# Performance work log

Hardware: AMD Instinct MI355X
Metric: run time of the kernel (lower is better)

Reference implementation:

```python
import jax, jax.numpy as jnp
import numpy as np

B, F, D = 16384, 256, 128
H = [512, 256]
OUT = 8
VOCAB = 100000


def setup_inputs() -> dict:
    key = jax.random.key(0)
    ks = jax.random.split(key, 16)
    s = lambda k, *sh: jax.random.normal(k, sh, jnp.float32) * 0.05
    return dict(
        features=jax.random.normal(ks[0], (B, F), jnp.float32),
        ent_idx=jax.random.randint(ks[1], (B,), 0, VOCAB),
        target=jax.random.randint(ks[2], (B,), 0, OUT),
        Wf=s(ks[3], F, D), bf=jnp.zeros((D,), jnp.float32),
        Wu=s(ks[4], D, D), bu=jnp.zeros((D,), jnp.float32),
        w_cf=s(ks[5], D), w_fc=s(ks[6], D),
        w_ef=s(ks[7], D), w_fe=s(ks[8], D),
        b_c=jnp.zeros((1,), jnp.float32), b_e=jnp.zeros((1,), jnp.float32),
        head_tab=s(ks[9], VOCAB, D), ent_tab=s(ks[10], VOCAB, D),
        W0=s(ks[11], 2 * D, H[0]), b0=jnp.zeros((H[0],), jnp.float32),
        W1=s(ks[12], H[0], H[1]), b1=jnp.zeros((H[1],), jnp.float32),
        W2=s(ks[13], H[1], OUT), b2=jnp.zeros((OUT,), jnp.float32),
    )


def cross_compress(f, e, w_cf, w_fc, w_ef, w_fe, b_c, b_e):
    # torch code builds c = f (outer) e of shape (B,D,D) then matmuls a (D,1)
    # vector; algebraically (f e^T) w = f * (e . w), so we use the O(B*D) form.
    ew_cf = e @ w_cf  # (B,)
    fw_fc = f @ w_fc
    ew_ef = e @ w_ef
    fw_fe = f @ w_fe
    new_f = f * ew_cf[:, None] + e * fw_fc[:, None] + b_c
    new_e = f * ew_ef[:, None] + e * fw_fe[:, None] + b_e
    return new_f, new_e


def reference(features, ent_idx, target, Wf, bf, Wu, bu, w_cf, w_fc, w_ef,
              w_fe, b_c, b_e, head_tab, ent_tab, W0, b0, W1, b1, W2, b2):
    # 'rec' branch of CompanyOperationEvaluation.forward (eval mode, dropout=id)
    cf = jax.nn.relu(features @ Wf + bf)          # feature_layer
    e = ent_tab[ent_idx]                           # entity_embed lookup
    h = head_tab[ent_idx]                          # head_embed lookup (same ids)
    for _ in range(2):
        cf = jax.nn.relu(cf @ Wu + bu)             # user_low_mlp_layer
        h, e = cross_compress(h, e, w_cf, w_fc, w_ef, w_fe, b_c, b_e)
    high = jnp.concatenate([cf, e], axis=1)        # (B, 2D)
    x = jax.nn.relu(high @ W0 + b0)
    x = jax.nn.relu(x @ W1 + b1)
    x = jax.nn.relu(x @ W2 + b2)                   # pred_last_layer
    prob = jax.nn.softmax(x, axis=1)
    return (prob, target)
```

## Files before the change

### kernel.cpp

```cpp
#include <hip/hip_runtime.h>
#include <hip/hip_bf16.h>


typedef __bf16 bf16x8 __attribute__((ext_vector_type(8)));
typedef float floatx4 __attribute__((ext_vector_type(4)));

__device__ __forceinline__ unsigned short f2bf(float x) {
  unsigned int u = __builtin_bit_cast(unsigned int, x);
  u = (u + 0x7FFFu + ((u >> 16) & 1u)) >> 16;
  return (unsigned short)u;
}

__global__ __launch_bounds__(256) void prep_kernel(
    const int* __restrict__ ent_idx, const float* __restrict__ head_tab,
    const float* __restrict__ ent_tab,
    const float* __restrict__ w_cf, const float* __restrict__ w_fc,
    const float* __restrict__ w_ef, const float* __restrict__ w_fe,
    const float* __restrict__ b_c, const float* __restrict__ b_e,
    const float* __restrict__ Wf, const float* __restrict__ Wu,
    const float* __restrict__ W0, const float* __restrict__ W1,
    const float* __restrict__ W2,
    unsigned short* __restrict__ high,
    unsigned short* __restrict__ wfT, unsigned short* __restrict__ wuT,
    unsigned short* __restrict__ w0T, unsigned short* __restrict__ w1T,
    unsigned short* __restrict__ w2T) {
  __shared__ unsigned short tile[32][34];
  const int bid = blockIdx.x, tid = threadIdx.x;
  if (bid < 2048) {
    const int row = bid * 8 + (tid >> 5);
    const int c = (tid & 31) * 4;
    const int idx = ent_idx[row];
    float4 hv = *(const float4*)(head_tab + (size_t)idx * 128 + c);
    float4 ev = *(const float4*)(ent_tab + (size_t)idx * 128 + c);
    float h[4] = {hv.x, hv.y, hv.z, hv.w};
    float e[4] = {ev.x, ev.y, ev.z, ev.w};
    float wcf[4], wfc[4], wef[4], wfe[4];
#pragma unroll
    for (int j = 0; j < 4; ++j) {
      wcf[j] = w_cf[c + j]; wfc[j] = w_fc[c + j];
      wef[j] = w_ef[c + j]; wfe[j] = w_fe[c + j];
    }
    const float bc = b_c[0], be = b_e[0];
#pragma unroll
    for (int it = 0; it < 2; ++it) {
      float d0 = 0, d1 = 0, d2 = 0, d3 = 0;
#pragma unroll
      for (int j = 0; j < 4; ++j) {
        d0 += e[j] * wcf[j]; d1 += h[j] * wfc[j];
        d2 += e[j] * wef[j]; d3 += h[j] * wfe[j];
      }
#pragma unroll
      for (int s = 1; s < 32; s <<= 1) {
        d0 += __shfl_xor(d0, s); d1 += __shfl_xor(d1, s);
        d2 += __shfl_xor(d2, s); d3 += __shfl_xor(d3, s);
      }
      float nh[4], ne[4];
#pragma unroll
      for (int j = 0; j < 4; ++j) {
        nh[j] = h[j] * d0 + e[j] * d1 + bc;
        ne[j] = h[j] * d2 + e[j] * d3 + be;
      }
#pragma unroll
      for (int j = 0; j < 4; ++j) { h[j] = nh[j]; e[j] = ne[j]; }
    }
    uint2 v;
    v.x = (unsigned)f2bf(e[0]) | ((unsigned)f2bf(e[1]) << 16);
    v.y = (unsigned)f2bf(e[2]) | ((unsigned)f2bf(e[3]) << 16);
    *(uint2*)(high + (size_t)row * 256 + 128 + c) = v;
  } else if (bid < 2352) {
    int t = bid - 2048;
    const float* src; unsigned short* dst; int N, K, kt, nt;
    if (t < 32)       { src = Wf; dst = wfT; N = 128; K = 256; kt = t >> 2;       nt = t & 3; }
    else if (t < 48)  { t -= 32;  src = Wu; dst = wuT; N = 128; K = 128; kt = t >> 2; nt = t & 3; }
    else if (t < 176) { t -= 48;  src = W0; dst = w0T; N = 512; K = 256; kt = t >> 4; nt = t & 15; }
    else              { t -= 176; src = W1; dst = w1T; N = 256; K = 512; kt = t >> 3; nt = t & 7; }
    {
      int r = tid >> 3, cg = (tid & 7) * 4;
      float4 v = *(const float4*)(src + (size_t)(kt * 32 + r) * N + nt * 32 + cg);
      tile[r][cg + 0] = f2bf(v.x); tile[r][cg + 1] = f2bf(v.y);
      tile[r][cg + 2] = f2bf(v.z); tile[r][cg + 3] = f2bf(v.w);
    }
    __syncthreads();
    {
      int rp = tid >> 3, cg = (tid & 7) * 4;
      uint2 o;
      o.x = (unsigned)tile[cg + 0][rp] | ((unsigned)tile[cg + 1][rp] << 16);
      o.y = (unsigned)tile[cg + 2][rp] | ((unsigned)tile[cg + 3][rp] << 16);
      *(uint2*)(dst + (size_t)(nt * 32 + rp) * K + kt * 32 + cg) = o;
    }
  } else {
#pragma unroll
    for (int i = 0; i < 8; ++i) {
      int g = tid * 8 + i, k = g >> 3, n = g & 7;
      w2T[n * 256 + k] = f2bf(W2[g]);
    }
  }
}

template <int LDA>
__device__ __forceinline__ void layer_acc(const unsigned short* A_sh,
                                          const unsigned short* __restrict__ BT,
                                          int K, unsigned short* b_sh,
                                          floatx4 acc[2][4]) {
  const int tid = threadIdx.x, lane = tid & 63, wave = tid >> 6;
  const int wm = wave >> 1, wn = wave & 1;
  const int m16 = lane & 15, quad = lane >> 4;
#pragma unroll
  for (int mi = 0; mi < 2; ++mi)
#pragma unroll
    for (int ni = 0; ni < 4; ++ni) acc[mi][ni] = (floatx4){0.f, 0.f, 0.f, 0.f};
  for (int k0 = 0; k0 < K; k0 += 64) {
    __syncthreads();
#pragma unroll
    for (int i = 0; i < 4; ++i) {
      int chunk = i * 256 + tid;
      int row = chunk >> 3, seg = chunk & 7;
      *(uint4*)&b_sh[row * 72 + seg * 8] =
          *(const uint4*)(BT + (size_t)row * K + k0 + seg * 8);
    }
    __syncthreads();
#pragma unroll
    for (int kk = 0; kk < 64; kk += 32) {
      bf16x8 a[2], b[4];
#pragma unroll
      for (int mi = 0; mi < 2; ++mi)
        a[mi] = *(const bf16x8*)&A_sh[(wm * 32 + mi * 16 + m16) * LDA + k0 + kk + quad * 8];
#pragma unroll
      for (int ni = 0; ni < 4; ++ni)
        b[ni] = *(const bf16x8*)&b_sh[(wn * 64 + ni * 16 + m16) * 72 + kk + quad * 8];
#pragma unroll
      for (int mi = 0; mi < 2; ++mi)
#pragma unroll
        for (int ni = 0; ni < 4; ++ni)
          acc[mi][ni] = __builtin_amdgcn_mfma_f32_16x16x32_bf16(a[mi], b[ni], acc[mi][ni], 0, 0, 0);
    }
  }
  __syncthreads();
}

__global__ __launch_bounds__(256) void cf_chain_kernel(
    const float* __restrict__ features, const unsigned short* __restrict__ wfT,
    const unsigned short* __restrict__ wuT, const float* __restrict__ bf_,
    const float* __restrict__ bu, unsigned short* __restrict__ high) {
  __shared__ __align__(16) unsigned short feat_sh[64 * 264];
  __shared__ __align__(16) unsigned short buf0[64 * 136];
  __shared__ __align__(16) unsigned short buf1[64 * 136];
  __shared__ __align__(16) unsigned short b_sh[128 * 72];
  const int tid = threadIdx.x;
  const int r0 = blockIdx.x * 64;
#pragma unroll
  for (int i = 0; i < 16; ++i) {
    int row = i * 4 + (tid >> 6);
    int c = (tid & 63) * 4;
    float4 v = *(const float4*)(features + (size_t)(r0 + row) * 256 + c);
    uint2 o;
    o.x = (unsigned)f2bf(v.x) | ((unsigned)f2bf(v.y) << 16);
    o.y = (unsigned)f2bf(v.z) | ((unsigned)f2bf(v.w) << 16);
    *(uint2*)&feat_sh[row * 264 + c] = o;
  }
  const int lane = tid & 63, wave = tid >> 6;
  const int wm = wave >> 1, wn = wave & 1;
  const int m16 = lane & 15, quad = lane >> 4;
  floatx4 acc[2][4];

  layer_acc<264>(feat_sh, wfT, 256, b_sh, acc);
#pragma unroll
  for (int mi = 0; mi < 2; ++mi)
#pragma unroll
    for (int ni = 0; ni < 4; ++ni) {
      int col = wn * 64 + ni * 16 + m16;
      float bv = bf_[col];
#pragma unroll
      for (int r = 0; r < 4; ++r)
        buf0[(wm * 32 + mi * 16 + quad * 4 + r) * 136 + col] =
            f2bf(fmaxf(acc[mi][ni][r] + bv, 0.f));
    }
  layer_acc<136>(buf0, wuT, 128, b_sh, acc);
#pragma unroll
  for (int mi = 0; mi < 2; ++mi)
#pragma unroll
    for (int ni = 0; ni < 4; ++ni) {
      int col = wn * 64 + ni * 16 + m16;
      float bv = bu[col];
#pragma unroll
      for (int r = 0; r < 4; ++r)
        buf1[(wm * 32 + mi * 16 + quad * 4 + r) * 136 + col] =
            f2bf(fmaxf(acc[mi][ni][r] + bv, 0.f));
    }
  layer_acc<136>(buf1, wuT, 128, b_sh, acc);
#pragma unroll
  for (int mi = 0; mi < 2; ++mi)
#pragma unroll
    for (int ni = 0; ni < 4; ++ni) {
      int col = wn * 64 + ni * 16 + m16;
      float bv = bu[col];
#pragma unroll
      for (int r = 0; r < 4; ++r) {
        int row = r0 + wm * 32 + mi * 16 + quad * 4 + r;
        high[(size_t)row * 256 + col] = f2bf(fmaxf(acc[mi][ni][r] + bv, 0.f));
      }
    }
}

__global__ __launch_bounds__(256) void gemm_kernel(
    const unsigned short* __restrict__ A, const unsigned short* __restrict__ BT,
    const float* __restrict__ bias, unsigned short* __restrict__ C,
    int K, int ldc) {
  __shared__ __align__(16) unsigned short a_sh[128 * 72];
  __shared__ __align__(16) unsigned short b_sh[64 * 72];
  const int tid = threadIdx.x;
  const int bn = blockIdx.x, bm = blockIdx.y;
  const int lane = tid & 63;
  const int wave = tid >> 6;
  const int wm = wave & 1, wn = wave >> 1;
  const int m16 = lane & 15, quad = lane >> 4;

  floatx4 acc[4][2];
#pragma unroll
  for (int i = 0; i < 4; ++i)
#pragma unroll
    for (int j = 0; j < 2; ++j) acc[i][j] = (floatx4){0.f, 0.f, 0.f, 0.f};

  for (int k0 = 0; k0 < K; k0 += 64) {
#pragma unroll
    for (int i = 0; i < 4; ++i) {
      int chunk = i * 256 + tid;
      int row = chunk >> 3, seg = chunk & 7;
      *(uint4*)&a_sh[row * 72 + seg * 8] =
          *(const uint4*)(A + (size_t)(bm * 128 + row) * K + k0 + seg * 8);
    }
#pragma unroll
    for (int i = 0; i < 2; ++i) {
      int chunk = i * 256 + tid;
      int row = chunk >> 3, seg = chunk & 7;
      *(uint4*)&b_sh[row * 72 + seg * 8] =
          *(const uint4*)(BT + (size_t)(bn * 64 + row) * K + k0 + seg * 8);
    }
    __syncthreads();
#pragma unroll
    for (int kk = 0; kk < 64; kk += 32) {
      bf16x8 af[4], bfr[2];
#pragma unroll
      for (int mi = 0; mi < 4; ++mi)
        af[mi] = *(const bf16x8*)&a_sh[(wm * 64 + mi * 16 + m16) * 72 + kk + quad * 8];
#pragma unroll
      for (int ni = 0; ni < 2; ++ni)
        bfr[ni] = *(const bf16x8*)&b_sh[(wn * 32 + ni * 16 + m16) * 72 + kk + quad * 8];
#pragma unroll
      for (int mi = 0; mi < 4; ++mi)
#pragma unroll
        for (int ni = 0; ni < 2; ++ni)
          acc[mi][ni] = __builtin_amdgcn_mfma_f32_16x16x32_bf16(
              af[mi], bfr[ni], acc[mi][ni], 0, 0, 0);
    }
    __syncthreads();
  }
#pragma unroll
  for (int mi = 0; mi < 4; ++mi) {
#pragma unroll
    for (int ni = 0; ni < 2; ++ni) {
      int col = bn * 64 + wn * 32 + ni * 16 + m16;
      float bv = bias[col];
#pragma unroll
      for (int r = 0; r < 4; ++r) {
        int row = bm * 128 + wm * 64 + mi * 16 + quad * 4 + r;
        float v = fmaxf(acc[mi][ni][r] + bv, 0.f);
        C[(size_t)row * ldc + col] = f2bf(v);
      }
    }
  }
}

__global__ __launch_bounds__(256) void gemm_w1_final_kernel(
    const unsigned short* __restrict__ x0, const unsigned short* __restrict__ w1T,
    const float* __restrict__ b1, const unsigned short* __restrict__ w2T,
    const float* __restrict__ b2, const int* __restrict__ target,
    float* __restrict__ out) {
  __shared__ __align__(16) unsigned short a_sh[64 * 72];
  __shared__ __align__(16) unsigned short b_sh[256 * 72];
  __shared__ __align__(16) unsigned short x1_sh[64 * 264];
  __shared__ __align__(16) unsigned short w2_sh[2048];
  const int tid = threadIdx.x;
  const int r0 = blockIdx.x * 64;
  *(uint4*)&w2_sh[tid * 8] = *(const uint4*)(w2T + tid * 8);
  const int lane = tid & 63, wave = tid >> 6;
  const int m16 = lane & 15, quad = lane >> 4;
  floatx4 acc[4][4];
#pragma unroll
  for (int mi = 0; mi < 4; ++mi)
#pragma unroll
    for (int ni = 0; ni < 4; ++ni) acc[mi][ni] = (floatx4){0.f, 0.f, 0.f, 0.f};

  for (int k0 = 0; k0 < 512; k0 += 64) {
    __syncthreads();
#pragma unroll
    for (int i = 0; i < 2; ++i) {
      int chunk = i * 256 + tid;
      int row = chunk >> 3, seg = chunk & 7;
      *(uint4*)&a_sh[row * 72 + seg * 8] =
          *(const uint4*)(x0 + (size_t)(r0 + row) * 512 + k0 + seg * 8);
    }
#pragma unroll
    for (int i = 0; i < 8; ++i) {
      int chunk = i * 256 + tid;
      int row = chunk >> 3, seg = chunk & 7;
      *(uint4*)&b_sh[row * 72 + seg * 8] =
          *(const uint4*)(w1T + (size_t)row * 512 + k0 + seg * 8);
    }
    __syncthreads();
#pragma unroll
    for (int kk = 0; kk < 64; kk += 32) {
      bf16x8 a[4], b[4];
#pragma unroll
      for (int mi = 0; mi < 4; ++mi)
        a[mi] = *(const bf16x8*)&a_sh[(mi * 16 + m16) * 72 + kk + quad * 8];
#pragma unroll
      for (int ni = 0; ni < 4; ++ni)
        b[ni] = *(const bf16x8*)&b_sh[(wave * 64 + ni * 16 + m16) * 72 + kk + quad * 8];
#pragma unroll
      for (int mi = 0; mi < 4; ++mi)
#pragma unroll
        for (int ni = 0; ni < 4; ++ni)
          acc[mi][ni] = __builtin_amdgcn_mfma_f32_16x16x32_bf16(a[mi], b[ni], acc[mi][ni], 0, 0, 0);
    }
  }
#pragma unroll
  for (int mi = 0; mi < 4; ++mi)
#pragma unroll
    for (int ni = 0; ni < 4; ++ni) {
      int col = wave * 64 + ni * 16 + m16;
      float bv = b1[col];
#pragma unroll
      for (int r = 0; r < 4; ++r)
        x1_sh[(mi * 16 + quad * 4 + r) * 264 + col] = f2bf(fmaxf(acc[mi][ni][r] + bv, 0.f));
    }
  __syncthreads();
  {
    int row = tid >> 2, q = tid & 3;
    float p[8];
#pragma unroll
    for (int n = 0; n < 8; ++n) p[n] = 0.f;
#pragma unroll
    for (int jb = 0; jb < 8; ++jb) {
      bf16x8 xv = *(const bf16x8*)&x1_sh[row * 264 + q * 64 + jb * 8];
#pragma unroll
      for (int n = 0; n < 8; ++n) {
        bf16x8 wv = *(const bf16x8*)&w2_sh[n * 256 + q * 64 + jb * 8];
#pragma unroll
        for (int j = 0; j < 8; ++j) p[n] += (float)xv[j] * (float)wv[j];
      }
    }
#pragma unroll
    for (int s = 1; s < 4; s <<= 1)
#pragma unroll
      for (int n = 0; n < 8; ++n) p[n] += __shfl_xor(p[n], s);
    if (q == 0) {
      float mx = -1e30f;
#pragma unroll
      for (int n = 0; n < 8; ++n) {
        p[n] = fmaxf(p[n] + b2[n], 0.f);
        mx = fmaxf(mx, p[n]);
      }
      float sum = 0.f;
#pragma unroll
      for (int n = 0; n < 8; ++n) { p[n] = __expf(p[n] - mx); sum += p[n]; }
      const float inv = 1.f / sum;
      const int gr = r0 + row;
      float4 o0 = {p[0] * inv, p[1] * inv, p[2] * inv, p[3] * inv};
      float4 o1 = {p[4] * inv, p[5] * inv, p[6] * inv, p[7] * inv};
      *(float4*)(out + (size_t)gr * 8) = o0;
      *(float4*)(out + (size_t)gr * 8 + 4) = o1;
      out[16384 * 8 + gr] = (float)target[gr];
    }
  }
}

extern "C" void kernel_launch(void* const* d_in, const int* in_sizes, int n_in,
                              void* d_out, int out_size, void* d_ws, size_t ws_size,
                              hipStream_t stream) {
  const float* features = (const float*)d_in[0];
  const int* ent_idx    = (const int*)d_in[1];
  const int* target     = (const int*)d_in[2];
  const float* Wf  = (const float*)d_in[3];
  const float* bf_ = (const float*)d_in[4];
  const float* Wu  = (const float*)d_in[5];
  const float* bu  = (const float*)d_in[6];
  const float* w_cf = (const float*)d_in[7];
  const float* w_fc = (const float*)d_in[8];
  const float* w_ef = (const float*)d_in[9];
  const float* w_fe = (const float*)d_in[10];
  const float* b_c  = (const float*)d_in[11];
  const float* b_e  = (const float*)d_in[12];
  const float* head_tab = (const float*)d_in[13];
  const float* ent_tab  = (const float*)d_in[14];
  const float* W0 = (const float*)d_in[15];
  const float* b0 = (const float*)d_in[16];
  const float* W1 = (const float*)d_in[17];
  const float* b1 = (const float*)d_in[18];
  const float* W2 = (const float*)d_in[19];
  const float* b2 = (const float*)d_in[20];
  float* out = (float*)d_out;

  unsigned short* ws = (unsigned short*)d_ws;
  size_t off = 0;
  auto alloc = [&](size_t n) { unsigned short* p = ws + off; off += n; return p; };
  unsigned short* high = alloc(16384ull * 256);
  unsigned short* x0   = alloc(16384ull * 512);
  unsigned short* wfT  = alloc(32768);
  unsigned short* wuT  = alloc(16384);
  unsigned short* w0T  = alloc(131072);
  unsigned short* w1T  = alloc(131072);
  unsigned short* w2T  = alloc(2048);
  (void)ws_size; (void)in_sizes; (void)n_in; (void)out_size;

  prep_kernel<<<2353, 256, 0, stream>>>(ent_idx, head_tab, ent_tab,
      w_cf, w_fc, w_ef, w_fe, b_c, b_e, Wf, Wu, W0, W1, W2,
      high, wfT, wuT, w0T, w1T, w2T);
  cf_chain_kernel<<<256, 256, 0, stream>>>(features, wfT, wuT, bf_, bu, high);
  gemm_kernel<<<dim3(8, 128), 256, 0, stream>>>(high, w0T, b0, x0, 256, 512);
  gemm_w1_final_kernel<<<256, 256, 0, stream>>>(x0, w1T, b1, w2T, b2, target, out);
}
```

Measured before the change: 196.5 us.

## Retile MLP kernels: 32-row blocks for chain and final, 128x128 GEMM tiles

The cf chain and final W1/W2 kernels now process 32 rows per block instead of 64, which doubles the grid to 512 blocks so the 256-CU GPU gets more parallelism. The final kernel reuses the B staging buffer for x1 to cut LDS use. The W0 GEMM switches from 128x64 to 128x128 tiles to improve operand reuse, at the cost of halving its grid to 512 blocks. The trade-off is that smaller row tiles reload the weights more often per row, while the larger GEMM tile needs more registers.

```diff
diff --git a/kernel.cpp b/kernel.cpp
--- a/kernel.cpp
+++ b/kernel.cpp
@@ -98,17 +98,16 @@
 }
 
 template <int LDA>
-__device__ __forceinline__ void layer_acc(const unsigned short* A_sh,
-                                          const unsigned short* __restrict__ BT,
-                                          int K, unsigned short* b_sh,
-                                          floatx4 acc[2][4]) {
+__device__ __forceinline__ void layer32(const unsigned short* A_sh,
+                                        const unsigned short* __restrict__ BT,
+                                        int K, unsigned short* b_sh,
+                                        floatx4 acc[2][2]) {
   const int tid = threadIdx.x, lane = tid & 63, wave = tid >> 6;
-  const int wm = wave >> 1, wn = wave & 1;
   const int m16 = lane & 15, quad = lane >> 4;
 #pragma unroll
   for (int mi = 0; mi < 2; ++mi)
 #pragma unroll
-    for (int ni = 0; ni < 4; ++ni) acc[mi][ni] = (floatx4){0.f, 0.f, 0.f, 0.f};
+    for (int ni = 0; ni < 2; ++ni) acc[mi][ni] = (floatx4){0.f, 0.f, 0.f, 0.f};
   for (int k0 = 0; k0 < K; k0 += 64) {
     __syncthreads();
 #pragma unroll
@@ -121,17 +120,17 @@
     __syncthreads();
 #pragma unroll
     for (int kk = 0; kk < 64; kk += 32) {
-      bf16x8 a[2], b[4];
+      bf16x8 a[2], b[2];
 #pragma unroll
       for (int mi = 0; mi < 2; ++mi)
-        a[mi] = *(const bf16x8*)&A_sh[(wm * 32 + mi * 16 + m16) * LDA + k0 + kk + quad * 8];
-#pragma unroll
-      for (int ni = 0; ni < 4; ++ni)
-        b[ni] = *(const bf16x8*)&b_sh[(wn * 64 + ni * 16 + m16) * 72 + kk + quad * 8];
+        a[mi] = *(const bf16x8*)&A_sh[(mi * 16 + m16) * LDA + k0 + kk + quad * 8];
+#pragma unroll
+      for (int ni = 0; ni < 2; ++ni)
+        b[ni] = *(const bf16x8*)&b_sh[(wave * 32 + ni * 16 + m16) * 72 + kk + quad * 8];
 #pragma unroll
       for (int mi = 0; mi < 2; ++mi)
 #pragma unroll
-        for (int ni = 0; ni < 4; ++ni)
+        for (int ni = 0; ni < 2; ++ni)
           acc[mi][ni] = __builtin_amdgcn_mfma_f32_16x16x32_bf16(a[mi], b[ni], acc[mi][ni], 0, 0, 0);
     }
   }
@@ -142,16 +141,16 @@
     const float* __restrict__ features, const unsigned short* __restrict__ wfT,
     const unsigned short* __restrict__ wuT, const float* __restrict__ bf_,
     const float* __restrict__ bu, unsigned short* __restrict__ high) {
-  __shared__ __align__(16) unsigned short feat_sh[64 * 264];
-  __shared__ __align__(16) unsigned short buf0[64 * 136];
-  __shared__ __align__(16) unsigned short buf1[64 * 136];
+  __shared__ __align__(16) unsigned short feat_sh[32 * 264];
+  __shared__ __align__(16) unsigned short buf0[32 * 136];
+  __shared__ __align__(16) unsigned short buf1[32 * 136];
   __shared__ __align__(16) unsigned short b_sh[128 * 72];
   const int tid = threadIdx.x;
-  const int r0 = blockIdx.x * 64;
-#pragma unroll
-  for (int i = 0; i < 16; ++i) {
-    int row = i * 4 + (tid >> 6);
-    int c = (tid & 63) * 4;
+  const int r0 = blockIdx.x * 32;
+#pragma unroll
+  for (int i = 0; i < 8; ++i) {
+    int idx = i * 256 + tid;
+    int row = idx >> 6, c = (idx & 63) * 4;
     float4 v = *(const float4*)(features + (size_t)(r0 + row) * 256 + c);
     uint2 o;
     o.x = (unsigned)f2bf(v.x) | ((unsigned)f2bf(v.y) << 16);
@@ -159,55 +158,54 @@
     *(uint2*)&feat_sh[row * 264 + c] = o;
   }
   const int lane = tid & 63, wave = tid >> 6;
-  const int wm = wave >> 1, wn = wave & 1;
   const int m16 = lane & 15, quad = lane >> 4;
-  floatx4 acc[2][4];
-
-  layer_acc<264>(feat_sh, wfT, 256, b_sh, acc);
-#pragma unroll
-  for (int mi = 0; mi < 2; ++mi)
-#pragma unroll
-    for (int ni = 0; ni < 4; ++ni) {
-      int col = wn * 64 + ni * 16 + m16;
+  floatx4 acc[2][2];
+
+  layer32<264>(feat_sh, wfT, 256, b_sh, acc);
+#pragma unroll
+  for (int mi = 0; mi < 2; ++mi)
+#pragma unroll
+    for (int ni = 0; ni < 2; ++ni) {
+      int col = wave * 32 + ni * 16 + m16;
       float bv = bf_[col];
 #pragma unroll
       for (int r = 0; r < 4; ++r)
-        buf0[(wm * 32 + mi * 16 + quad * 4 + r) * 136 + col] =
+        buf0[(mi * 16 + quad * 4 + r) * 136 + col] =
             f2bf(fmaxf(acc[mi][ni][r] + bv, 0.f));
     }
-  layer_acc<136>(buf0, wuT, 128, b_sh, acc);
-#pragma unroll
-  for (int mi = 0; mi < 2; ++mi)
-#pragma unroll
-    for (int ni = 0; ni < 4; ++ni) {
-      int col = wn * 64 + ni * 16 + m16;
+  layer32<136>(buf0, wuT, 128, b_sh, acc);
+#pragma unroll
+  for (int mi = 0; mi < 2; ++mi)
+#pragma unroll
+    for (int ni = 0; ni < 2; ++ni) {
+      int col = wave * 32 + ni * 16 + m16;
       float bv = bu[col];
 #pragma unroll
       for (int r = 0; r < 4; ++r)
-        buf1[(wm * 32 + mi * 16 + quad * 4 + r) * 136 + col] =
+        buf1[(mi * 16 + quad * 4 + r) * 136 + col] =
             f2bf(fmaxf(acc[mi][ni][r] + bv, 0.f));
     }
-  layer_acc<136>(buf1, wuT, 128, b_sh, acc);
-#pragma unroll
-  for (int mi = 0; mi < 2; ++mi)
-#pragma unroll
-    for (int ni = 0; ni < 4; ++ni) {
-      int col = wn * 64 + ni * 16 + m16;
+  layer32<136>(buf1, wuT, 128, b_sh, acc);
+#pragma unroll
+  for (int mi = 0; mi < 2; ++mi)
+#pragma unroll
+    for (int ni = 0; ni < 2; ++ni) {
+      int col = wave * 32 + ni * 16 + m16;
       float bv = bu[col];
 #pragma unroll
       for (int r = 0; r < 4; ++r) {
-        int row = r0 + wm * 32 + mi * 16 + quad * 4 + r;
+        int row = r0 + mi * 16 + quad * 4 + r;
         high[(size_t)row * 256 + col] = f2bf(fmaxf(acc[mi][ni][r] + bv, 0.f));
       }
     }
 }
 
-__global__ __launch_bounds__(256) void gemm_kernel(
+__global__ __launch_bounds__(256) void gemm128_kernel(
     const unsigned short* __restrict__ A, const unsigned short* __restrict__ BT,
     const float* __restrict__ bias, unsigned short* __restrict__ C,
     int K, int ldc) {
   __shared__ __align__(16) unsigned short a_sh[128 * 72];
-  __shared__ __align__(16) unsigned short b_sh[64 * 72];
+  __shared__ __align__(16) unsigned short b_sh[128 * 72];
   const int tid = threadIdx.x;
   const int bn = blockIdx.x, bm = blockIdx.y;
   const int lane = tid & 63;
@@ -215,57 +213,51 @@
   const int wm = wave & 1, wn = wave >> 1;
   const int m16 = lane & 15, quad = lane >> 4;
 
-  floatx4 acc[4][2];
+  floatx4 acc[4][4];
 #pragma unroll
   for (int i = 0; i < 4; ++i)
 #pragma unroll
-    for (int j = 0; j < 2; ++j) acc[i][j] = (floatx4){0.f, 0.f, 0.f, 0.f};
+    for (int j = 0; j < 4; ++j) acc[i][j] = (floatx4){0.f, 0.f, 0.f, 0.f};
 
   for (int k0 = 0; k0 < K; k0 += 64) {
+    __syncthreads();
 #pragma unroll
     for (int i = 0; i < 4; ++i) {
       int chunk = i * 256 + tid;
       int row = chunk >> 3, seg = chunk & 7;
       *(uint4*)&a_sh[row * 72 + seg * 8] =
           *(const uint4*)(A + (size_t)(bm * 128 + row) * K + k0 + seg * 8);
-    }
-#pragma unroll
-    for (int i = 0; i < 2; ++i) {
-      int chunk = i * 256 + tid;
-      int row = chunk >> 3, seg = chunk & 7;
       *(uint4*)&b_sh[row * 72 + seg * 8] =
-          *(const uint4*)(BT + (size_t)(bn * 64 + row) * K + k0 + seg * 8);
+          *(const uint4*)(BT + (size_t)(bn * 128 + row) * K + k0 + seg * 8);
     }
     __syncthreads();
 #pragma unroll
     for (int kk = 0; kk < 64; kk += 32) {
-      bf16x8 af[4], bfr[2];
+      bf16x8 af[4], bfr[4];
 #pragma unroll
       for (int mi = 0; mi < 4; ++mi)
         af[mi] = *(const bf16x8*)&a_sh[(wm * 64 + mi * 16 + m16) * 72 + kk + quad * 8];
 #pragma unroll
-      for (int ni = 0; ni < 2; ++ni)
-        bfr[ni] = *(const bf16x8*)&b_sh[(wn * 32 + ni * 16 + m16) * 72 + kk + quad * 8];
+      for (int ni = 0; ni < 4; ++ni)
+        bfr[ni] = *(const bf16x8*)&b_sh[(wn * 64 + ni * 16 + m16) * 72 + kk + quad * 8];
 #pragma unroll
       for (int mi = 0; mi < 4; ++mi)
 #pragma unroll
-        for (int ni = 0; ni < 2; ++ni)
+        for (int ni = 0; ni < 4; ++ni)
           acc[mi][ni] = __builtin_amdgcn_mfma_f32_16x16x32_bf16(
               af[mi], bfr[ni], acc[mi][ni], 0, 0, 0);
     }
-    __syncthreads();
   }
 #pragma unroll
   for (int mi = 0; mi < 4; ++mi) {
 #pragma unroll
-    for (int ni = 0; ni < 2; ++ni) {
-      int col = bn * 64 + wn * 32 + ni * 16 + m16;
+    for (int ni = 0; ni < 4; ++ni) {
+      int col = bn * 128 + wn * 64 + ni * 16 + m16;
       float bv = bias[col];
 #pragma unroll
       for (int r = 0; r < 4; ++r) {
         int row = bm * 128 + wm * 64 + mi * 16 + quad * 4 + r;
-        float v = fmaxf(acc[mi][ni][r] + bv, 0.f);
-        C[(size_t)row * ldc + col] = f2bf(v);
+        C[(size_t)row * ldc + col] = f2bf(fmaxf(acc[mi][ni][r] + bv, 0.f));
       }
     }
   }
@@ -276,27 +268,25 @@
     const float* __restrict__ b1, const unsigned short* __restrict__ w2T,
     const float* __restrict__ b2, const int* __restrict__ target,
     float* __restrict__ out) {
-  __shared__ __align__(16) unsigned short a_sh[64 * 72];
+  __shared__ __align__(16) unsigned short a_sh[32 * 72];
   __shared__ __align__(16) unsigned short b_sh[256 * 72];
-  __shared__ __align__(16) unsigned short x1_sh[64 * 264];
   __shared__ __align__(16) unsigned short w2_sh[2048];
+  unsigned short* x1_sh = b_sh;
   const int tid = threadIdx.x;
-  const int r0 = blockIdx.x * 64;
+  const int r0 = blockIdx.x * 32;
   *(uint4*)&w2_sh[tid * 8] = *(const uint4*)(w2T + tid * 8);
   const int lane = tid & 63, wave = tid >> 6;
   const int m16 = lane & 15, quad = lane >> 4;
-  floatx4 acc[4][4];
-#pragma unroll
-  for (int mi = 0; mi < 4; ++mi)
+  floatx4 acc[2][4];
+#pragma unroll
+  for (int mi = 0; mi < 2; ++mi)
 #pragma unroll
     for (int ni = 0; ni < 4; ++ni) acc[mi][ni] = (floatx4){0.f, 0.f, 0.f, 0.f};
 
   for (int k0 = 0; k0 < 512; k0 += 64) {
     __syncthreads();
-#pragma unroll
-    for (int i = 0; i < 2; ++i) {
-      int chunk = i * 256 + tid;
-      int row = chunk >> 3, seg = chunk & 7;
+    {
+      int row = tid >> 3, seg = tid & 7;
       *(uint4*)&a_sh[row * 72 + seg * 8] =
           *(const uint4*)(x0 + (size_t)(r0 + row) * 512 + k0 + seg * 8);
     }
@@ -310,22 +300,23 @@
     __syncthreads();
 #pragma unroll
     for (int kk = 0; kk < 64; kk += 32) {
-      bf16x8 a[4], b[4];
-#pragma unroll
-      for (int mi = 0; mi < 4; ++mi)
+      bf16x8 a[2], b[4];
+#pragma unroll
+      for (int mi = 0; mi < 2; ++mi)
         a[mi] = *(const bf16x8*)&a_sh[(mi * 16 + m16) * 72 + kk + quad * 8];
 #pragma unroll
       for (int ni = 0; ni < 4; ++ni)
         b[ni] = *(const bf16x8*)&b_sh[(wave * 64 + ni * 16 + m16) * 72 + kk + quad * 8];
 #pragma unroll
-      for (int mi = 0; mi < 4; ++mi)
+      for (int mi = 0; mi < 2; ++mi)
 #pragma unroll
         for (int ni = 0; ni < 4; ++ni)
           acc[mi][ni] = __builtin_amdgcn_mfma_f32_16x16x32_bf16(a[mi], b[ni], acc[mi][ni], 0, 0, 0);
     }
   }
-#pragma unroll
-  for (int mi = 0; mi < 4; ++mi)
+  __syncthreads();
+#pragma unroll
+  for (int mi = 0; mi < 2; ++mi)
 #pragma unroll
     for (int ni = 0; ni < 4; ++ni) {
       int col = wave * 64 + ni * 16 + m16;
@@ -336,22 +327,22 @@
     }
   __syncthreads();
   {
-    int row = tid >> 2, q = tid & 3;
+    int row = tid >> 3, q = tid & 7;
     float p[8];
 #pragma unroll
     for (int n = 0; n < 8; ++n) p[n] = 0.f;
 #pragma unroll
-    for (int jb = 0; jb < 8; ++jb) {
-      bf16x8 xv = *(const bf16x8*)&x1_sh[row * 264 + q * 64 + jb * 8];
+    for (int jb = 0; jb < 4; ++jb) {
+      bf16x8 xv = *(const bf16x8*)&x1_sh[row * 264 + q * 32 + jb * 8];
 #pragma unroll
       for (int n = 0; n < 8; ++n) {
-        bf16x8 wv = *(const bf16x8*)&w2_sh[n * 256 + q * 64 + jb * 8];
+        bf16x8 wv = *(const bf16x8*)&w2_sh[n * 256 + q * 32 + jb * 8];
 #pragma unroll
         for (int j = 0; j < 8; ++j) p[n] += (float)xv[j] * (float)wv[j];
       }
     }
 #pragma unroll
-    for (int s = 1; s < 4; s <<= 1)
+    for (int s = 1; s < 8; s <<= 1)
 #pragma unroll
       for (int n = 0; n < 8; ++n) p[n] += __shfl_xor(p[n], s);
     if (q == 0) {
@@ -416,7 +407,7 @@
   prep_kernel<<<2353, 256, 0, stream>>>(ent_idx, head_tab, ent_tab,
       w_cf, w_fc, w_ef, w_fe, b_c, b_e, Wf, Wu, W0, W1, W2,
       high, wfT, wuT, w0T, w1T, w2T);
-  cf_chain_kernel<<<256, 256, 0, stream>>>(features, wfT, wuT, bf_, bu, high);
-  gemm_kernel<<<dim3(8, 128), 256, 0, stream>>>(high, w0T, b0, x0, 256, 512);
-  gemm_w1_final_kernel<<<256, 256, 0, stream>>>(x0, w1T, b1, w2T, b2, target, out);
-}
+  cf_chain_kernel<<<512, 256, 0, stream>>>(features, wfT, wuT, bf_, bu, high);
+  gemm128_kernel<<<dim3(4, 128), 256, 0, stream>>>(high, w0T, b0, x0, 256, 512);
+  gemm_w1_final_kernel<<<512, 256, 0, stream>>>(x0, w1T, b1, w2T, b2, target, out);
+}
```

Result: faster. 191.6 us (-2.5%).

## Fuse embedding cross-compress into cf chain, widen W0 GEMM tile, reuse LDS

Applied to the files above, without the earlier changes.

Moves the embedding gather and cross-compress work out of the prep kernel into the cf_chain kernel, so prep only transposes weights and runs far fewer blocks. Widens the W0 GEMM tile from 128x64 to 128x128, halving the number of blocks and re-reading A fewer times. Aliases shared-memory buffers (buf1 onto feat_sh, x1_sh onto b_sh) to cut LDS use per block, which may allow more blocks per CU, at the cost of extra synchronisation and larger per-thread accumulator state.

```diff
diff --git a/kernel.cpp b/kernel.cpp
--- a/kernel.cpp
+++ b/kernel.cpp
@@ -12,63 +12,16 @@
 }
 
 __global__ __launch_bounds__(256) void prep_kernel(
-    const int* __restrict__ ent_idx, const float* __restrict__ head_tab,
-    const float* __restrict__ ent_tab,
-    const float* __restrict__ w_cf, const float* __restrict__ w_fc,
-    const float* __restrict__ w_ef, const float* __restrict__ w_fe,
-    const float* __restrict__ b_c, const float* __restrict__ b_e,
     const float* __restrict__ Wf, const float* __restrict__ Wu,
     const float* __restrict__ W0, const float* __restrict__ W1,
     const float* __restrict__ W2,
-    unsigned short* __restrict__ high,
     unsigned short* __restrict__ wfT, unsigned short* __restrict__ wuT,
     unsigned short* __restrict__ w0T, unsigned short* __restrict__ w1T,
     unsigned short* __restrict__ w2T) {
   __shared__ unsigned short tile[32][34];
   const int bid = blockIdx.x, tid = threadIdx.x;
-  if (bid < 2048) {
-    const int row = bid * 8 + (tid >> 5);
-    const int c = (tid & 31) * 4;
-    const int idx = ent_idx[row];
-    float4 hv = *(const float4*)(head_tab + (size_t)idx * 128 + c);
-    float4 ev = *(const float4*)(ent_tab + (size_t)idx * 128 + c);
-    float h[4] = {hv.x, hv.y, hv.z, hv.w};
-    float e[4] = {ev.x, ev.y, ev.z, ev.w};
-    float wcf[4], wfc[4], wef[4], wfe[4];
-#pragma unroll
-    for (int j = 0; j < 4; ++j) {
-      wcf[j] = w_cf[c + j]; wfc[j] = w_fc[c + j];
-      wef[j] = w_ef[c + j]; wfe[j] = w_fe[c + j];
-    }
-    const float bc = b_c[0], be = b_e[0];
-#pragma unroll
-    for (int it = 0; it < 2; ++it) {
-      float d0 = 0, d1 = 0, d2 = 0, d3 = 0;
-#pragma unroll
-      for (int j = 0; j < 4; ++j) {
-        d0 += e[j] * wcf[j]; d1 += h[j] * wfc[j];
-        d2 += e[j] * wef[j]; d3 += h[j] * wfe[j];
-      }
-#pragma unroll
-      for (int s = 1; s < 32; s <<= 1) {
-        d0 += __shfl_xor(d0, s); d1 += __shfl_xor(d1, s);
-        d2 += __shfl_xor(d2, s); d3 += __shfl_xor(d3, s);
-      }
-      float nh[4], ne[4];
-#pragma unroll
-      for (int j = 0; j < 4; ++j) {
-        nh[j] = h[j] * d0 + e[j] * d1 + bc;
-        ne[j] = h[j] * d2 + e[j] * d3 + be;
-      }
-#pragma unroll
-      for (int j = 0; j < 4; ++j) { h[j] = nh[j]; e[j] = ne[j]; }
-    }
-    uint2 v;
-    v.x = (unsigned)f2bf(e[0]) | ((unsigned)f2bf(e[1]) << 16);
-    v.y = (unsigned)f2bf(e[2]) | ((unsigned)f2bf(e[3]) << 16);
-    *(uint2*)(high + (size_t)row * 256 + 128 + c) = v;
-  } else if (bid < 2352) {
-    int t = bid - 2048;
+  if (bid < 304) {
+    int t = bid;
     const float* src; unsigned short* dst; int N, K, kt, nt;
     if (t < 32)       { src = Wf; dst = wfT; N = 128; K = 256; kt = t >> 2;       nt = t & 3; }
     else if (t < 48)  { t -= 32;  src = Wu; dst = wuT; N = 128; K = 128; kt = t >> 2; nt = t & 3; }
@@ -97,11 +50,10 @@
   }
 }
 
-template <int LDA>
-__device__ __forceinline__ void layer_acc(const unsigned short* A_sh,
-                                          const unsigned short* __restrict__ BT,
-                                          int K, unsigned short* b_sh,
-                                          floatx4 acc[2][4]) {
+template <int K, int LDA, int LDB>
+__device__ __forceinline__ void gemm_64x128(
+    const unsigned short* A_sh, const unsigned short* __restrict__ BT,
+    unsigned short* b_sh, floatx4 acc[2][4]) {
   const int tid = threadIdx.x, lane = tid & 63, wave = tid >> 6;
   const int wm = wave >> 1, wn = wave & 1;
   const int m16 = lane & 15, quad = lane >> 4;
@@ -116,7 +68,7 @@
       int chunk = i * 256 + tid;
       int row = chunk >> 3, seg = chunk & 7;
       *(uint4*)&b_sh[row * 72 + seg * 8] =
-          *(const uint4*)(BT + (size_t)row * K + k0 + seg * 8);
+          *(const uint4*)(BT + (size_t)row * LDB + k0 + seg * 8);
     }
     __syncthreads();
 #pragma unroll
@@ -138,44 +90,122 @@
   __syncthreads();
 }
 
+__device__ __forceinline__ void epi64(const floatx4 acc[2][4],
+                                      const float* __restrict__ bias,
+                                      unsigned short* dst, int ldd) {
+  const int lane = threadIdx.x & 63, wave = threadIdx.x >> 6;
+  const int wm = wave >> 1, wn = wave & 1;
+  const int m16 = lane & 15, quad = lane >> 4;
+#pragma unroll
+  for (int mi = 0; mi < 2; ++mi)
+#pragma unroll
+    for (int ni = 0; ni < 4; ++ni) {
+      int col = wn * 64 + ni * 16 + m16;
+      float bv = bias[col];
+#pragma unroll
+      for (int r = 0; r < 4; ++r)
+        dst[(wm * 32 + mi * 16 + quad * 4 + r) * ldd + col] =
+            f2bf(fmaxf(acc[mi][ni][r] + bv, 0.f));
+    }
+}
+
 __global__ __launch_bounds__(256) void cf_chain_kernel(
-    const float* __restrict__ features, const unsigned short* __restrict__ wfT,
-    const unsigned short* __restrict__ wuT, const float* __restrict__ bf_,
-    const float* __restrict__ bu, unsigned short* __restrict__ high) {
+    const float* __restrict__ features, const int* __restrict__ ent_idx,
+    const float* __restrict__ head_tab, const float* __restrict__ ent_tab,
+    const float* __restrict__ w_cf, const float* __restrict__ w_fc,
+    const float* __restrict__ w_ef, const float* __restrict__ w_fe,
+    const float* __restrict__ b_c, const float* __restrict__ b_e,
+    const unsigned short* __restrict__ wfT, const unsigned short* __restrict__ wuT,
+    const float* __restrict__ bf_, const float* __restrict__ bu,
+    unsigned short* __restrict__ high) {
   __shared__ __align__(16) unsigned short feat_sh[64 * 264];
   __shared__ __align__(16) unsigned short buf0[64 * 136];
-  __shared__ __align__(16) unsigned short buf1[64 * 136];
   __shared__ __align__(16) unsigned short b_sh[128 * 72];
+  unsigned short* buf1 = feat_sh;
   const int tid = threadIdx.x;
   const int r0 = blockIdx.x * 64;
+
 #pragma unroll
   for (int i = 0; i < 16; ++i) {
-    int row = i * 4 + (tid >> 6);
-    int c = (tid & 63) * 4;
+    int idx4 = i * 256 + tid;
+    int row = idx4 >> 6, c = (idx4 & 63) * 4;
     float4 v = *(const float4*)(features + (size_t)(r0 + row) * 256 + c);
     uint2 o;
     o.x = (unsigned)f2bf(v.x) | ((unsigned)f2bf(v.y) << 16);
     o.y = (unsigned)f2bf(v.z) | ((unsigned)f2bf(v.w) << 16);
     *(uint2*)&feat_sh[row * 264 + c] = o;
   }
+
+  {
+    const float bc = b_c[0], be = b_e[0];
+#pragma unroll
+    for (int p = 0; p < 4; ++p) {
+      const int rl = p * 16 + (tid >> 4);
+      const int c = (tid & 15) * 8;
+      const int idx = ent_idx[r0 + rl];
+      float h[8], e[8], wcf[8], wfc[8], wef[8], wfe[8];
+      {
+        float4 t0 = *(const float4*)(head_tab + (size_t)idx * 128 + c);
+        float4 t1 = *(const float4*)(head_tab + (size_t)idx * 128 + c + 4);
+        h[0]=t0.x; h[1]=t0.y; h[2]=t0.z; h[3]=t0.w;
+        h[4]=t1.x; h[5]=t1.y; h[6]=t1.z; h[7]=t1.w;
+        t0 = *(const float4*)(ent_tab + (size_t)idx * 128 + c);
+        t1 = *(const float4*)(ent_tab + (size_t)idx * 128 + c + 4);
+        e[0]=t0.x; e[1]=t0.y; e[2]=t0.z; e[3]=t0.w;
+        e[4]=t1.x; e[5]=t1.y; e[6]=t1.z; e[7]=t1.w;
+        t0 = *(const float4*)(w_cf + c); t1 = *(const float4*)(w_cf + c + 4);
+        wcf[0]=t0.x; wcf[1]=t0.y; wcf[2]=t0.z; wcf[3]=t0.w;
+        wcf[4]=t1.x; wcf[5]=t1.y; wcf[6]=t1.z; wcf[7]=t1.w;
+        t0 = *(const float4*)(w_fc + c); t1 = *(const float4*)(w_fc + c + 4);
+        wfc[0]=t0.x; wfc[1]=t0.y; wfc[2]=t0.z; wfc[3]=t0.w;
+        wfc[4]=t1.x; wfc[5]=t1.y; wfc[6]=t1.z; wfc[7]=t1.w;
+        t0 = *(const float4*)(w_ef + c); t1 = *(const float4*)(w_ef + c + 4);
+        wef[0]=t0.x; wef[1]=t0.y; wef[2]=t0.z; wef[3]=t0.w;
+        wef[4]=t1.x; wef[5]=t1.y; wef[6]=t1.z; wef[7]=t1.w;
+        t0 = *(const float4*)(w_fe + c); t1 = *(const float4*)(w_fe + c + 4);
+        wfe[0]=t0.x; wfe[1]=t0.y; wfe[2]=t0.z; wfe[3]=t0.w;
+        wfe[4]=t1.x; wfe[5]=t1.y; wfe[6]=t1.z; wfe[7]=t1.w;
+      }
+#pragma unroll
+      for (int it = 0; it < 2; ++it) {
+        float d0 = 0, d1 = 0, d2 = 0, d3 = 0;
+#pragma unroll
+        for (int j = 0; j < 8; ++j) {
+          d0 += e[j] * wcf[j]; d1 += h[j] * wfc[j];
+          d2 += e[j] * wef[j]; d3 += h[j] * wfe[j];
+        }
+#pragma unroll
+        for (int s = 1; s < 16; s <<= 1) {
+          d0 += __shfl_xor(d0, s); d1 += __shfl_xor(d1, s);
+          d2 += __shfl_xor(d2, s); d3 += __shfl_xor(d3, s);
+        }
+        float nh2[8], ne2[8];
+#pragma unroll
+        for (int j = 0; j < 8; ++j) {
+          nh2[j] = h[j] * d0 + e[j] * d1 + bc;
+          ne2[j] = h[j] * d2 + e[j] * d3 + be;
+        }
+#pragma unroll
+        for (int j = 0; j < 8; ++j) { h[j] = nh2[j]; e[j] = ne2[j]; }
+      }
+      uint4 v;
+      v.x = (unsigned)f2bf(e[0]) | ((unsigned)f2bf(e[1]) << 16);
+      v.y = (unsigned)f2bf(e[2]) | ((unsigned)f2bf(e[3]) << 16);
+      v.z = (unsigned)f2bf(e[4]) | ((unsigned)f2bf(e[5]) << 16);
+      v.w = (unsigned)f2bf(e[6]) | ((unsigned)f2bf(e[7]) << 16);
+      *(uint4*)(high + (size_t)(r0 + rl) * 256 + 128 + c) = v;
+    }
+  }
+
+  floatx4 acc[2][4];
   const int lane = tid & 63, wave = tid >> 6;
   const int wm = wave >> 1, wn = wave & 1;
   const int m16 = lane & 15, quad = lane >> 4;
-  floatx4 acc[2][4];
-
-  layer_acc<264>(feat_sh, wfT, 256, b_sh, acc);
-#pragma unroll
-  for (int mi = 0; mi < 2; ++mi)
-#pragma unroll
-    for (int ni = 0; ni < 4; ++ni) {
-      int col = wn * 64 + ni * 16 + m16;
-      float bv = bf_[col];
-#pragma unroll
-      for (int r = 0; r < 4; ++r)
-        buf0[(wm * 32 + mi * 16 + quad * 4 + r) * 136 + col] =
-            f2bf(fmaxf(acc[mi][ni][r] + bv, 0.f));
-    }
-  layer_acc<136>(buf0, wuT, 128, b_sh, acc);
+  gemm_64x128<256, 264, 256>(feat_sh, wfT, b_sh, acc);
+  epi64(acc, bf_, buf0, 136);
+  gemm_64x128<128, 136, 128>(buf0, wuT, b_sh, acc);
+  epi64(acc, bu, buf1, 136);
+  gemm_64x128<128, 136, 128>(buf1, wuT, b_sh, acc);
 #pragma unroll
   for (int mi = 0; mi < 2; ++mi)
 #pragma unroll
@@ -183,18 +213,6 @@
       int col = wn * 64 + ni * 16 + m16;
       float bv = bu[col];
 #pragma unroll
-      for (int r = 0; r < 4; ++r)
-        buf1[(wm * 32 + mi * 16 + quad * 4 + r) * 136 + col] =
-            f2bf(fmaxf(acc[mi][ni][r] + bv, 0.f));
-    }
-  layer_acc<136>(buf1, wuT, 128, b_sh, acc);
-#pragma unroll
-  for (int mi = 0; mi < 2; ++mi)
-#pragma unroll
-    for (int ni = 0; ni < 4; ++ni) {
-      int col = wn * 64 + ni * 16 + m16;
-      float bv = bu[col];
-#pragma unroll
       for (int r = 0; r < 4; ++r) {
         int row = r0 + wm * 32 + mi * 16 + quad * 4 + r;
         high[(size_t)row * 256 + col] = f2bf(fmaxf(acc[mi][ni][r] + bv, 0.f));
@@ -202,12 +220,12 @@
     }
 }
 
-__global__ __launch_bounds__(256) void gemm_kernel(
+__global__ __launch_bounds__(256) void gemm128_kernel(
     const unsigned short* __restrict__ A, const unsigned short* __restrict__ BT,
     const float* __restrict__ bias, unsigned short* __restrict__ C,
     int K, int ldc) {
   __shared__ __align__(16) unsigned short a_sh[128 * 72];
-  __shared__ __align__(16) unsigned short b_sh[64 * 72];
+  __shared__ __align__(16) unsigned short b_sh[128 * 72];
   const int tid = threadIdx.x;
   const int bn = blockIdx.x, bm = blockIdx.y;
   const int lane = tid & 63;
@@ -215,57 +233,51 @@
   const int wm = wave & 1, wn = wave >> 1;
   const int m16 = lane & 15, quad = lane >> 4;
 
-  floatx4 acc[4][2];
+  floatx4 acc[4][4];
 #pragma unroll
   for (int i = 0; i < 4; ++i)
 #pragma unroll
-    for (int j = 0; j < 2; ++j) acc[i][j] = (floatx4){0.f, 0.f, 0.f, 0.f};
+    for (int j = 0; j < 4; ++j) acc[i][j] = (floatx4){0.f, 0.f, 0.f, 0.f};
 
   for (int k0 = 0; k0 < K; k0 += 64) {
+    __syncthreads();
 #pragma unroll
     for (int i = 0; i < 4; ++i) {
       int chunk = i * 256 + tid;
       int row = chunk >> 3, seg = chunk & 7;
       *(uint4*)&a_sh[row * 72 + seg * 8] =
           *(const uint4*)(A + (size_t)(bm * 128 + row) * K + k0 + seg * 8);
-    }
-#pragma unroll
-    for (int i = 0; i < 2; ++i) {
-      int chunk = i * 256 + tid;
-      int row = chunk >> 3, seg = chunk & 7;
       *(uint4*)&b_sh[row * 72 + seg * 8] =
-          *(const uint4*)(BT + (size_t)(bn * 64 + row) * K + k0 + seg * 8);
+          *(const uint4*)(BT + (size_t)(bn * 128 + row) * K + k0 + seg * 8);
     }
     __syncthreads();
 #pragma unroll
     for (int kk = 0; kk < 64; kk += 32) {
-      bf16x8 af[4], bfr[2];
+      bf16x8 af[4], bfr[4];
 #pragma unroll
       for (int mi = 0; mi < 4; ++mi)
         af[mi] = *(const bf16x8*)&a_sh[(wm * 64 + mi * 16 + m16) * 72 + kk + quad * 8];
 #pragma unroll
-      for (int ni = 0; ni < 2; ++ni)
-        bfr[ni] = *(const bf16x8*)&b_sh[(wn * 32 + ni * 16 + m16) * 72 + kk + quad * 8];
+      for (int ni = 0; ni < 4; ++ni)
+        bfr[ni] = *(const bf16x8*)&b_sh[(wn * 64 + ni * 16 + m16) * 72 + kk + quad * 8];
 #pragma unroll
       for (int mi = 0; mi < 4; ++mi)
 #pragma unroll
-        for (int ni = 0; ni < 2; ++ni)
+        for (int ni = 0; ni < 4; ++ni)
           acc[mi][ni] = __builtin_amdgcn_mfma_f32_16x16x32_bf16(
               af[mi], bfr[ni], acc[mi][ni], 0, 0, 0);
     }
-    __syncthreads();
   }
 #pragma unroll
   for (int mi = 0; mi < 4; ++mi) {
 #pragma unroll
-    for (int ni = 0; ni < 2; ++ni) {
-      int col = bn * 64 + wn * 32 + ni * 16 + m16;
+    for (int ni = 0; ni < 4; ++ni) {
+      int col = bn * 128 + wn * 64 + ni * 16 + m16;
       float bv = bias[col];
 #pragma unroll
       for (int r = 0; r < 4; ++r) {
         int row = bm * 128 + wm * 64 + mi * 16 + quad * 4 + r;
-        float v = fmaxf(acc[mi][ni][r] + bv, 0.f);
-        C[(size_t)row * ldc + col] = f2bf(v);
+        C[(size_t)row * ldc + col] = f2bf(fmaxf(acc[mi][ni][r] + bv, 0.f));
       }
     }
   }
@@ -278,8 +290,8 @@
     float* __restrict__ out) {
   __shared__ __align__(16) unsigned short a_sh[64 * 72];
   __shared__ __align__(16) unsigned short b_sh[256 * 72];
-  __shared__ __align__(16) unsigned short x1_sh[64 * 264];
   __shared__ __align__(16) unsigned short w2_sh[2048];
+  unsigned short* x1_sh = b_sh;
   const int tid = threadIdx.x;
   const int r0 = blockIdx.x * 64;
   *(uint4*)&w2_sh[tid * 8] = *(const uint4*)(w2T + tid * 8);
@@ -324,6 +336,7 @@
           acc[mi][ni] = __builtin_amdgcn_mfma_f32_16x16x32_bf16(a[mi], b[ni], acc[mi][ni], 0, 0, 0);
     }
   }
+  __syncthreads();
 #pragma unroll
   for (int mi = 0; mi < 4; ++mi)
 #pragma unroll
@@ -413,10 +426,10 @@
   unsigned short* w2T  = alloc(2048);
   (void)ws_size; (void)in_sizes; (void)n_in; (void)out_size;
 
-  prep_kernel<<<2353, 256, 0, stream>>>(ent_idx, head_tab, ent_tab,
-      w_cf, w_fc, w_ef, w_fe, b_c, b_e, Wf, Wu, W0, W1, W2,
-      high, wfT, wuT, w0T, w1T, w2T);
-  cf_chain_kernel<<<256, 256, 0, stream>>>(features, wfT, wuT, bf_, bu, high);
-  gemm_kernel<<<dim3(8, 128), 256, 0, stream>>>(high, w0T, b0, x0, 256, 512);
+  prep_kernel<<<305, 256, 0, stream>>>(Wf, Wu, W0, W1, W2,
+                                       wfT, wuT, w0T, w1T, w2T);
+  cf_chain_kernel<<<256, 256, 0, stream>>>(features, ent_idx, head_tab,
+      ent_tab, w_cf, w_fc, w_ef, w_fe, b_c, b_e, wfT, wuT, bf_, bu, high);
+  gemm128_kernel<<<dim3(4, 128), 256, 0, stream>>>(high, w0T, b0, x0, 256, 512);
   gemm_w1_final_kernel<<<256, 256, 0, stream>>>(x0, w1T, b1, w2T, b2, target, out);
 }
```

New measurement: 192.4 us. 1.02x faster.
